# Kernel tuning notes

Measured on AMD Instinct MI355X. Metric: run time of the kernel, lower is better.

## Reference

```python
import jax, jax.numpy as jnp
import numpy as np

N, K, F = 20000, 32, 128
H, D = 4, 64            # heads, att_out_size
C = 40                  # num_classes
NEG_SLOPE = 0.2


def setup_inputs() -> dict:
    key = jax.random.key(0)
    ks = jax.random.split(key, 6)
    return {
        "node_feature": jax.random.normal(ks[0], (N, F), dtype=jnp.float32),
        "neighbor_nodes_feature": jax.random.normal(ks[1], (N, K, F), dtype=jnp.float32),
        "W": jax.random.normal(ks[2], (F, H * D), dtype=jnp.float32) / np.sqrt(F),
        "a_src": jax.random.normal(ks[3], (H, D), dtype=jnp.float32) / np.sqrt(D),
        "a_dst": jax.random.normal(ks[4], (H, D), dtype=jnp.float32) / np.sqrt(D),
        "weight": jax.random.normal(ks[5], (H * D, C), dtype=jnp.float32) / np.sqrt(H * D),
    }


def reference(node_feature, neighbor_nodes_feature, W, a_src, a_dst, weight):
    n = node_feature.shape[0]
    # Linear transform center nodes and neighbors, split heads
    h_i = (node_feature @ W).reshape(n, H, D)                     # [N,H,D]
    h_j = (neighbor_nodes_feature @ W).reshape(n, K, H, D)        # [N,K,H,D]
    # Attention logits: a_src . h_i + a_dst . h_j, LeakyReLU
    e_i = jnp.einsum('nhd,hd->nh', h_i, a_src)                    # [N,H]
    e_j = jnp.einsum('nkhd,hd->nkh', h_j, a_dst)                  # [N,K,H]
    e = jax.nn.leaky_relu(e_i[:, None, :] + e_j, NEG_SLOPE)       # [N,K,H]
    # Softmax over the K neighbors (segment softmax in dense form)
    alpha = jax.nn.softmax(e, axis=1)                             # [N,K,H]
    # Attention-weighted aggregation, concat heads
    out = jnp.einsum('nkh,nkhd->nhd', alpha, h_j).reshape(n, H * D)
    # Dense classifier (torch.mm)
    return out @ weight                                            # [N,C]
```

## Files before the change

kernel.cpp:

```cpp
#include <hip/hip_runtime.h>

#define KN 32
#define NF 128
#define NH 4
#define HD 256
#define NC 40
#define NPB 8
#define XSS 132

#define WS_WSRC 0
#define WS_WDST 512
#define WS_MT   1024

__global__ void gat_prep_wm(const float* __restrict__ W,
                            const float* __restrict__ a_src,
                            const float* __restrict__ a_dst,
                            const float* __restrict__ cls_w,
                            float* __restrict__ ws)
{
    if (blockIdx.x < 4) {
        int g = blockIdx.x * 256 + threadIdx.x;
        int which = g >> 9, h = (g >> 7) & 3, f = g & 127;
        const float* a = which ? a_dst : a_src;
        float s = 0.f;
        #pragma unroll 8
        for (int d = 0; d < 64; ++d)
            s = fmaf(W[f * HD + h * 64 + d], a[h * 64 + d], s);
        ws[g] = s;
    } else {
        int g = (blockIdx.x - 4) * 256 + threadIdx.x;
        if (g >= NC * 512) return;
        int cls = g >> 9, c = g & 511;
        int h = c >> 7, f = c & 127;
        float s = 0.f;
        #pragma unroll 8
        for (int d = 0; d < 64; ++d)
            s = fmaf(W[f * HD + h * 64 + d], cls_w[(h * 64 + d) * NC + cls], s);
        ws[WS_MT + (size_t)cls * 512 + c] = s;
    }
}

static __device__ __forceinline__ void lds_barrier() {
    __builtin_amdgcn_sched_barrier(0);
    asm volatile("s_waitcnt lgkmcnt(0)");
    __builtin_amdgcn_sched_barrier(0);
    __builtin_amdgcn_s_barrier();
    __builtin_amdgcn_sched_barrier(0);
}

__global__ __launch_bounds__(256, 3)
void gat_main(const float* __restrict__ nodef,
              const float* __restrict__ neigh,
              const float* __restrict__ ws,
              float* __restrict__ out, int n_nodes)
{
    __shared__ __align__(16) float Xs[2][KN * XSS];
    __shared__ __align__(16) float zl[NPB][512];
    __shared__ __align__(16) float e_lds[2][NH * KN];
    __shared__ __align__(16) float ei_lds[NPB][NH];

    const int t    = threadIdx.x;
    const int lane = t & 63;
    const int kq   = t >> 3;
    const int fq   = t & 7;
    const int wv   = t >> 6;
    const float* wsrc = ws + WS_WSRC;
    const float* wdst = ws + WS_WDST;
    const float* MT   = ws + WS_MT;

    const int node0 = blockIdx.x * NPB;
    if (node0 >= n_nodes) return;

    {
        const int i2 = t >> 5, sub = t & 31;
        float4 x = ((const float4*)(nodef + (size_t)(node0 + i2) * NF))[sub];
        float4 w0 = *(const float4*)&wsrc[0 * NF + sub * 4];
        float4 w1 = *(const float4*)&wsrc[1 * NF + sub * 4];
        float4 w2 = *(const float4*)&wsrc[2 * NF + sub * 4];
        float4 w3 = *(const float4*)&wsrc[3 * NF + sub * 4];
        float p0 = x.x*w0.x + x.y*w0.y + x.z*w0.z + x.w*w0.w;
        float p1 = x.x*w1.x + x.y*w1.y + x.z*w1.z + x.w*w1.w;
        float p2 = x.x*w2.x + x.y*w2.y + x.z*w2.z + x.w*w2.w;
        float p3 = x.x*w3.x + x.y*w3.y + x.z*w3.z + x.w*w3.w;
        #pragma unroll
        for (int st = 1; st < 32; st <<= 1) {
            p0 += __shfl_xor(p0, st); p1 += __shfl_xor(p1, st);
            p2 += __shfl_xor(p2, st); p3 += __shfl_xor(p3, st);
        }
        if (sub == 0)
            *(float4*)&ei_lds[i2][0] = make_float4(p0, p1, p2, p3);
    }

    float4 wd[4][4];
    #pragma unroll
    for (int h = 0; h < 4; ++h)
        #pragma unroll
        for (int j = 0; j < 4; ++j)
            wd[h][j] = *(const float4*)&wdst[h * NF + fq * 4 + 32 * j];

    float4 xv[3][4];
    #pragma unroll
    for (int s = 0; s < 3; ++s) {
        const float4* src = (const float4*)(neigh + ((size_t)(node0 + s) * KN + kq) * NF);
        #pragma unroll
        for (int j = 0; j < 4; ++j) xv[s][j] = src[fq + 8 * j];
    }

    #pragma unroll
    for (int i = 0; i < NPB; ++i) {
        const int set = i % 3;
        const int buf = i & 1;

        #pragma unroll
        for (int j = 0; j < 4; ++j)
            *(float4*)&Xs[buf][kq * XSS + fq * 4 + 32 * j] = xv[set][j];

        float s0 = 0.f, s1 = 0.f, s2 = 0.f, s3 = 0.f;
        #pragma unroll
        for (int j = 0; j < 4; ++j) {
            float4 x = xv[set][j];
            s0 += x.x*wd[0][j].x + x.y*wd[0][j].y + x.z*wd[0][j].z + x.w*wd[0][j].w;
            s1 += x.x*wd[1][j].x + x.y*wd[1][j].y + x.z*wd[1][j].z + x.w*wd[1][j].w;
            s2 += x.x*wd[2][j].x + x.y*wd[2][j].y + x.z*wd[2][j].z + x.w*wd[2][j].w;
            s3 += x.x*wd[3][j].x + x.y*wd[3][j].y + x.z*wd[3][j].z + x.w*wd[3][j].w;
        }

        if (i + 3 < NPB) {
            const float4* src = (const float4*)(neigh + ((size_t)(node0 + i + 3) * KN + kq) * NF);
            #pragma unroll
            for (int j = 0; j < 4; ++j) xv[set][j] = src[fq + 8 * j];
        }

        #pragma unroll
        for (int st = 1; st < 8; st <<= 1) {
            s0 += __shfl_xor(s0, st); s1 += __shfl_xor(s1, st);
            s2 += __shfl_xor(s2, st); s3 += __shfl_xor(s3, st);
        }
        if (fq == 0) {
            e_lds[buf][0 * KN + kq] = s0; e_lds[buf][1 * KN + kq] = s1;
            e_lds[buf][2 * KN + kq] = s2; e_lds[buf][3 * KN + kq] = s3;
        }

        lds_barrier();

        const float ei_h = ei_lds[i][wv];
        float ss = 0.f, zx = 0.f, zy = 0.f;
        #pragma unroll
        for (int m = 0; m < 8; ++m) {
            float4 evm = *(const float4*)&e_lds[buf][wv * KN + m * 4];
            float el[4] = {evm.x, evm.y, evm.z, evm.w};
            #pragma unroll
            for (int kk = 0; kk < 4; ++kk) {
                float z_ = ei_h + el[kk];
                float l_ = fmaxf(z_, 0.2f * z_);
                float p_ = __expf(l_);
                ss += p_;
                float2 x2 = *(const float2*)&Xs[buf][(m * 4 + kk) * XSS + 2 * lane];
                zx = fmaf(p_, x2.x, zx);
                zy = fmaf(p_, x2.y, zy);
            }
        }
        float inv = 1.f / ss;
        *(float2*)&zl[i][wv * NF + 2 * lane] = make_float2(zx * inv, zy * inv);
    }
    __syncthreads();

    float* ypart = &Xs[0][0];
    {
        int cls = t & 63, s = t >> 6;
        if (cls < NC) {
            const float4* mp = (const float4*)&MT[(size_t)cls * 512 + s * 128];
            float acc[NPB];
            #pragma unroll
            for (int i = 0; i < NPB; ++i) acc[i] = 0.f;
            #pragma unroll 2
            for (int c4 = 0; c4 < 32; ++c4) {
                float4 mv = mp[c4];
                #pragma unroll
                for (int i = 0; i < NPB; ++i) {
                    float4 zv = *(const float4*)&zl[i][s * 128 + c4 * 4];
                    acc[i] += zv.x * mv.x + zv.y * mv.y + zv.z * mv.z + zv.w * mv.w;
                }
            }
            #pragma unroll
            for (int i = 0; i < NPB; ++i)
                ypart[s * (NPB * NC) + i * NC + cls] = acc[i];
        }
    }
    __syncthreads();
    #pragma unroll
    for (int rep = 0; rep < 2; ++rep) {
        int p = t + rep * 256;
        if (p < NPB * NC) {
            float y = ypart[p] + ypart[NPB * NC + p]
                    + ypart[2 * NPB * NC + p] + ypart[3 * NPB * NC + p];
            out[(size_t)node0 * NC + p] = y;
        }
    }
}

extern "C" void kernel_launch(void* const* d_in, const int* in_sizes, int n_in,
                              void* d_out, int out_size, void* d_ws, size_t ws_size,
                              hipStream_t stream) {
    const float* nodef = (const float*)d_in[0];
    const float* neigh = (const float*)d_in[1];
    const float* W     = (const float*)d_in[2];
    const float* a_src = (const float*)d_in[3];
    const float* a_dst = (const float*)d_in[4];
    const float* cls_w = (const float*)d_in[5];
    float* out = (float*)d_out;
    float* ws  = (float*)d_ws;

    const int n_nodes = in_sizes[0] / NF;

    hipLaunchKernelGGL(gat_prep_wm, dim3(4 + (NC * 512 + 255) / 256), dim3(256), 0, stream,
                       W, a_src, a_dst, cls_w, ws);
    hipLaunchKernelGGL(gat_main, dim3((n_nodes + NPB - 1) / NPB), dim3(256), 0, stream,
                       nodef, neigh, ws, out, n_nodes);
}
```

Measured before the change: 126.3 us.

## Process two nodes per iteration and compute softmax once per (head,k)

```diff
diff --git a/kernel.cpp b/kernel.cpp
--- a/kernel.cpp
+++ b/kernel.cpp
@@ -57,13 +57,12 @@
     __shared__ __align__(16) float Xs[2][KN * XSS];
     __shared__ __align__(16) float zl[NPB][512];
     __shared__ __align__(16) float e_lds[2][NH * KN];
+    __shared__ __align__(16) float alpha_l[2][KN * NH];
     __shared__ __align__(16) float ei_lds[NPB][NH];
 
-    const int t    = threadIdx.x;
-    const int lane = t & 63;
-    const int kq   = t >> 3;
-    const int fq   = t & 7;
-    const int wv   = t >> 6;
+    const int t  = threadIdx.x;
+    const int kq = t >> 3;
+    const int fq = t & 7;
     const float* wsrc = ws + WS_WSRC;
     const float* wdst = ws + WS_WDST;
     const float* MT   = ws + WS_MT;
@@ -98,70 +97,86 @@
         for (int j = 0; j < 4; ++j)
             wd[h][j] = *(const float4*)&wdst[h * NF + fq * 4 + 32 * j];
 
-    float4 xv[3][4];
+    float4 xvA[4], xvB[4];
+    {
+        const float4* sA = (const float4*)(neigh + ((size_t)node0 * KN + kq) * NF);
+        const float4* sB = (const float4*)(neigh + ((size_t)(node0 + 1) * KN + kq) * NF);
+        #pragma unroll
+        for (int j = 0; j < 4; ++j) { xvA[j] = sA[fq + 8 * j]; xvB[j] = sB[fq + 8 * j]; }
+    }
+
     #pragma unroll
-    for (int s = 0; s < 3; ++s) {
-        const float4* src = (const float4*)(neigh + ((size_t)(node0 + s) * KN + kq) * NF);
-        #pragma unroll
-        for (int j = 0; j < 4; ++j) xv[s][j] = src[fq + 8 * j];
-    }
-
-    #pragma unroll
-    for (int i = 0; i < NPB; ++i) {
-        const int set = i % 3;
-        const int buf = i & 1;
-
-        #pragma unroll
-        for (int j = 0; j < 4; ++j)
-            *(float4*)&Xs[buf][kq * XSS + fq * 4 + 32 * j] = xv[set][j];
-
-        float s0 = 0.f, s1 = 0.f, s2 = 0.f, s3 = 0.f;
+    for (int ip = 0; ip < NPB; ip += 2) {
+        if (ip) lds_barrier();
         #pragma unroll
         for (int j = 0; j < 4; ++j) {
-            float4 x = xv[set][j];
-            s0 += x.x*wd[0][j].x + x.y*wd[0][j].y + x.z*wd[0][j].z + x.w*wd[0][j].w;
-            s1 += x.x*wd[1][j].x + x.y*wd[1][j].y + x.z*wd[1][j].z + x.w*wd[1][j].w;
-            s2 += x.x*wd[2][j].x + x.y*wd[2][j].y + x.z*wd[2][j].z + x.w*wd[2][j].w;
-            s3 += x.x*wd[3][j].x + x.y*wd[3][j].y + x.z*wd[3][j].z + x.w*wd[3][j].w;
-        }
-
-        if (i + 3 < NPB) {
-            const float4* src = (const float4*)(neigh + ((size_t)(node0 + i + 3) * KN + kq) * NF);
-            #pragma unroll
-            for (int j = 0; j < 4; ++j) xv[set][j] = src[fq + 8 * j];
-        }
-
+            *(float4*)&Xs[0][kq * XSS + fq * 4 + 32 * j] = xvA[j];
+            *(float4*)&Xs[1][kq * XSS + fq * 4 + 32 * j] = xvB[j];
+        }
+        float sA0 = 0.f, sA1 = 0.f, sA2 = 0.f, sA3 = 0.f;
+        float sB0 = 0.f, sB1 = 0.f, sB2 = 0.f, sB3 = 0.f;
+        #pragma unroll
+        for (int j = 0; j < 4; ++j) {
+            float4 a = xvA[j], b = xvB[j];
+            sA0 += a.x*wd[0][j].x + a.y*wd[0][j].y + a.z*wd[0][j].z + a.w*wd[0][j].w;
+            sA1 += a.x*wd[1][j].x + a.y*wd[1][j].y + a.z*wd[1][j].z + a.w*wd[1][j].w;
+            sA2 += a.x*wd[2][j].x + a.y*wd[2][j].y + a.z*wd[2][j].z + a.w*wd[2][j].w;
+            sA3 += a.x*wd[3][j].x + a.y*wd[3][j].y + a.z*wd[3][j].z + a.w*wd[3][j].w;
+            sB0 += b.x*wd[0][j].x + b.y*wd[0][j].y + b.z*wd[0][j].z + b.w*wd[0][j].w;
+            sB1 += b.x*wd[1][j].x + b.y*wd[1][j].y + b.z*wd[1][j].z + b.w*wd[1][j].w;
+            sB2 += b.x*wd[2][j].x + b.y*wd[2][j].y + b.z*wd[2][j].z + b.w*wd[2][j].w;
+            sB3 += b.x*wd[3][j].x + b.y*wd[3][j].y + b.z*wd[3][j].z + b.w*wd[3][j].w;
+        }
+        if (ip + 2 < NPB) {
+            const float4* sA = (const float4*)(neigh + ((size_t)(node0 + ip + 2) * KN + kq) * NF);
+            const float4* sB = (const float4*)(neigh + ((size_t)(node0 + ip + 3) * KN + kq) * NF);
+            #pragma unroll
+            for (int j = 0; j < 4; ++j) { xvA[j] = sA[fq + 8 * j]; xvB[j] = sB[fq + 8 * j]; }
+        }
         #pragma unroll
         for (int st = 1; st < 8; st <<= 1) {
-            s0 += __shfl_xor(s0, st); s1 += __shfl_xor(s1, st);
-            s2 += __shfl_xor(s2, st); s3 += __shfl_xor(s3, st);
+            sA0 += __shfl_xor(sA0, st); sA1 += __shfl_xor(sA1, st);
+            sA2 += __shfl_xor(sA2, st); sA3 += __shfl_xor(sA3, st);
+            sB0 += __shfl_xor(sB0, st); sB1 += __shfl_xor(sB1, st);
+            sB2 += __shfl_xor(sB2, st); sB3 += __shfl_xor(sB3, st);
         }
         if (fq == 0) {
-            e_lds[buf][0 * KN + kq] = s0; e_lds[buf][1 * KN + kq] = s1;
-            e_lds[buf][2 * KN + kq] = s2; e_lds[buf][3 * KN + kq] = s3;
-        }
-
+            e_lds[0][0 * KN + kq] = sA0; e_lds[0][1 * KN + kq] = sA1;
+            e_lds[0][2 * KN + kq] = sA2; e_lds[0][3 * KN + kq] = sA3;
+            e_lds[1][0 * KN + kq] = sB0; e_lds[1][1 * KN + kq] = sB1;
+            e_lds[1][2 * KN + kq] = sB2; e_lds[1][3 * KN + kq] = sB3;
+        }
         lds_barrier();
 
-        const float ei_h = ei_lds[i][wv];
-        float ss = 0.f, zx = 0.f, zy = 0.f;
-        #pragma unroll
-        for (int m = 0; m < 8; ++m) {
-            float4 evm = *(const float4*)&e_lds[buf][wv * KN + m * 4];
-            float el[4] = {evm.x, evm.y, evm.z, evm.w};
-            #pragma unroll
-            for (int kk = 0; kk < 4; ++kk) {
-                float z_ = ei_h + el[kk];
-                float l_ = fmaxf(z_, 0.2f * z_);
-                float p_ = __expf(l_);
-                ss += p_;
-                float2 x2 = *(const float2*)&Xs[buf][(m * 4 + kk) * XSS + 2 * lane];
-                zx = fmaf(p_, x2.x, zx);
-                zy = fmaf(p_, x2.y, zy);
+        {
+            const int n = t >> 7, h = (t >> 5) & 3, k = t & 31;
+            float z = ei_lds[ip + n][h] + e_lds[n][h * KN + k];
+            float l = fmaxf(z, 0.2f * z);
+            float p = __expf(l);
+            float sm = p;
+            #pragma unroll
+            for (int st = 1; st < 32; st <<= 1) sm += __shfl_xor(sm, st);
+            alpha_l[n][k * 4 + h] = p / sm;
+        }
+        lds_barrier();
+
+        {
+            const int n = t >> 7, c = t & 127;
+            float z0 = 0.f, z1 = 0.f, z2 = 0.f, z3 = 0.f;
+            #pragma unroll 8
+            for (int k = 0; k < KN; ++k) {
+                float4 a4 = *(const float4*)&alpha_l[n][k * 4];
+                float  x  = Xs[n][k * XSS + c];
+                z0 = fmaf(a4.x, x, z0);
+                z1 = fmaf(a4.y, x, z1);
+                z2 = fmaf(a4.z, x, z2);
+                z3 = fmaf(a4.w, x, z3);
             }
-        }
-        float inv = 1.f / ss;
-        *(float2*)&zl[i][wv * NF + 2 * lane] = make_float2(zx * inv, zy * inv);
+            zl[ip + n][0 * NF + c] = z0;
+            zl[ip + n][1 * NF + c] = z1;
+            zl[ip + n][2 * NF + c] = z2;
+            zl[ip + n][3 * NF + c] = z3;
+        }
     }
     __syncthreads();
 
```

New measurement: 105.1 us. 16.8% less time.
